# Performance work log

Measured on AMD Instinct MI355X. Metric: run time of the kernel, lower is better.

The kernel has to match this reference:

```python
import jax, jax.numpy as jnp
import numpy as np

N = 50000       # nodes
E = 1200000     # edges (before self-loops)
IN_CH = 128
HID = 64
L = 3           # FAConv layers
EPS_RES = 0.1   # FAConv eps residual weight
BN_EPS = 1e-5


def _bn(x, g, b):
    # BatchNorm1d, training-mode statistics (biased variance, like torch)
    mu = x.mean(axis=0)
    var = x.var(axis=0)
    return g * (x - mu) * jax.lax.rsqrt(var + BN_EPS) + b


def setup_inputs() -> dict:
    key = jax.random.key(0)
    ks = jax.random.split(key, 12)
    s = lambda d: 1.0 / np.sqrt(d)
    H2 = HID // 2
    return {
        "x": jax.random.normal(ks[0], (N, IN_CH), jnp.float32),
        "edge_index": jax.random.randint(ks[1], (2, E), 0, N, dtype=jnp.int32),
        "batch_size": 10000,
        "W_in": jax.random.normal(ks[2], (IN_CH, HID), jnp.float32) * s(IN_CH),
        "b_in": jnp.zeros((HID,), jnp.float32),
        "att_l": jax.random.normal(ks[3], (L, HID), jnp.float32) * s(HID),
        "att_r": jax.random.normal(ks[4], (L, HID), jnp.float32) * s(HID),
        "bn_g": jnp.ones((L, HID), jnp.float32),
        "bn_b": jnp.zeros((L, HID), jnp.float32),
        "W1": jax.random.normal(ks[5], (HID, HID), jnp.float32) * s(HID),
        "b1": jnp.zeros((HID,), jnp.float32),
        "g1": jnp.ones((HID,), jnp.float32),
        "be1": jnp.zeros((HID,), jnp.float32),
        "W2": jax.random.normal(ks[6], (HID, H2), jnp.float32) * s(HID),
        "b2": jnp.zeros((H2,), jnp.float32),
        "g2": jnp.ones((H2,), jnp.float32),
        "be2": jnp.zeros((H2,), jnp.float32),
        "W3": jax.random.normal(ks[7], (H2, 1), jnp.float32) * s(H2),
        "b3": jnp.zeros((1,), jnp.float32),
    }


def reference(x, edge_index, batch_size, W_in, b_in, att_l, att_r, bn_g, bn_b,
              W1, b1, g1, be1, W2, b2, g2, be2, W3, b3):
    n = x.shape[0]
    # gcn_norm with self-loops (same for all layers since graph is fixed)
    loops = jnp.arange(n, dtype=edge_index.dtype)
    src = jnp.concatenate([edge_index[0], loops])  # j (source)
    dst = jnp.concatenate([edge_index[1], loops])  # i (target)
    deg = jax.ops.segment_sum(jnp.ones_like(dst, dtype=x.dtype), dst, num_segments=n)
    dinv = jnp.where(deg > 0, jax.lax.rsqrt(deg), 0.0)
    norm = dinv[src] * dinv[dst]                   # [E+N]

    x0 = jax.nn.relu(x @ W_in + b_in)              # [N, HID]
    h = x0
    for l in range(L):
        al = h @ att_l[l]                          # [N] att_l^T x
        ar = h @ att_r[l]                          # [N] att_r^T x
        alpha = jnp.tanh(al[src] + ar[dst])        # [E+N] signed attention
        msg = h[src] * (alpha * norm)[:, None]     # gather + weight
        out = jax.ops.segment_sum(msg, dst, num_segments=n) + EPS_RES * x0
        h = _bn(jax.nn.relu(out), bn_g[l], bn_b[l])

    z = h[:batch_size]
    z = jax.nn.relu(_bn(z @ W1 + b1, g1, be1))
    z = jax.nn.relu(_bn(z @ W2 + b2, g2, be2))
    return (z @ W3 + b3).squeeze(-1)
```

## Files before the change

kernel.cpp:

```cpp
#include <hip/hip_runtime.h>
#include <hip/hip_bf16.h>
#include <math.h>

#define NND 50000
#define NE  1200000
#define TOT (NE + NND)
#define INCH 128
#define HID 64
#define H2  32
#define NL  3
#define BSZ 10000
#define NB  196
#define NHB 128
#define NSTAT 128
#define NAGG 2048
#define CHUNK 4096
#define EPS_RES 0.1f
#define BN_EPS 1e-5f

typedef unsigned short ushort8v __attribute__((ext_vector_type(8)));
typedef unsigned short ushort4v __attribute__((ext_vector_type(4)));

__device__ __forceinline__ float b2f(unsigned short u) {
    return __uint_as_float((unsigned)u << 16);
}

__device__ __forceinline__ float fast_tanh(float x) {
    float cx = fminf(fmaxf(x, -8.f), 8.f);
    float e = __expf(2.f * cx);
    return 1.f - __fdividef(2.f, e + 1.f);
}


__global__ __launch_bounds__(256) void bhist_kernel(const int* __restrict__ dst, int* __restrict__ bh_part, int ne) {
    __shared__ int arr[256];
    arr[threadIdx.x] = 0;
    __syncthreads();
    int i = blockIdx.x * 256 + threadIdx.x;
    int stride = gridDim.x * 256;
    for (int e = i; e < ne; e += stride) atomicAdd(&arr[dst[e] >> 8], 1);
    __syncthreads();
    bh_part[blockIdx.x * 256 + threadIdx.x] = arr[threadIdx.x];
}

__global__ __launch_bounds__(256) void bscan_kernel(const int* __restrict__ bh_part,
                                                    int* __restrict__ bstart, int* __restrict__ bcur,
                                                    int* __restrict__ offsets) {
    __shared__ int ls[256];
    int t = threadIdx.x;
    int v = 0;
    for (int k = 0; k < NHB; k++) v += bh_part[k * 256 + t];
    ls[t] = v;
    __syncthreads();
    for (int off = 1; off < 256; off <<= 1) {
        int tv = (t >= off) ? ls[t - off] : 0;
        __syncthreads();
        ls[t] += tv;
        __syncthreads();
    }
    int excl = ls[t] - v;
    if (t < NB) { bstart[t] = excl; bcur[t] = excl; }
    if (t == NB) bstart[NB] = ls[NB - 1];
    if (t == 0) offsets[NND] = TOT;
}

__global__ __launch_bounds__(256) void passA_kernel(const int* __restrict__ src, const int* __restrict__ dst,
                                                    int* __restrict__ bcur, unsigned* __restrict__ ebuf, int ne) {
    __shared__ int arr[256];
    int t = threadIdx.x;
    int base = blockIdx.x * CHUNK;
    int lim = min(base + CHUNK, ne);
    arr[t] = 0;
    __syncthreads();
    for (int e = base + t; e < lim; e += 256) atomicAdd(&arr[dst[e] >> 8], 1);
    __syncthreads();
    int cnt_t = arr[t];
    int claimed = 0;
    if (cnt_t > 0) claimed = atomicAdd(&bcur[t], cnt_t);
    __syncthreads();
    arr[t] = claimed;
    __syncthreads();
    for (int e = base + t; e < lim; e += 256) {
        int d = dst[e];
        int pos = atomicAdd(&arr[d >> 8], 1);
        ebuf[pos] = ((unsigned)src[e] << 8) | (unsigned)(d & 255);
    }
}

__global__ __launch_bounds__(256) void bucket_build_kernel(const unsigned* __restrict__ ebuf, const int* __restrict__ bstart,
                                                           int* __restrict__ offsets, int* __restrict__ csr,
                                                           float* __restrict__ aldi_f) {
    __shared__ int dcnt[256];
    __shared__ int ls[256];
    __shared__ int cur[256];
    int b = blockIdx.x, t = threadIdx.x;
    dcnt[t] = 0;
    __syncthreads();
    int beg = bstart[b], end = bstart[b + 1];
    for (int p = beg + t; p < end; p += 256) atomicAdd(&dcnt[ebuf[p] & 255u], 1);
    __syncthreads();
    int node = b * 256 + t;
    bool valid = node < NND;
    int d = valid ? (dcnt[t] + 1) : 0;
    ls[t] = d;
    __syncthreads();
    for (int off = 1; off < 256; off <<= 1) {
        int tv = (t >= off) ? ls[t - off] : 0;
        __syncthreads();
        ls[t] += tv;
        __syncthreads();
    }
    int off = bstart[b] + b * 256 + ls[t] - d;
    if (valid) {
        offsets[node] = off;
        aldi_f[2 * node + 1] = rsqrtf((float)d);
        csr[off] = node;
        cur[t] = off + 1;
    }
    __syncthreads();
    for (int p = beg + t; p < end; p += 256) {
        unsigned ed = ebuf[p];
        int pos = atomicAdd(&cur[ed & 255u], 1);
        csr[pos] = (int)(ed >> 8);
    }
}

__global__ __launch_bounds__(256) void gemm_in_kernel(const float* __restrict__ x, const float* __restrict__ W,
                                                      const float* __restrict__ b,
                                                      const float* __restrict__ attl, const float* __restrict__ attr,
                                                      __hip_bfloat16* __restrict__ x0bf,
                                                      float* __restrict__ aldi_f, float* __restrict__ ar) {
    __shared__ float Wl[INCH * HID];
    __shared__ float xs[16 * INCH];
    int t = threadIdx.x;
    for (int i = t; i < INCH * HID; i += 256) Wl[i] = W[i];
    size_t rowbase = (size_t)blockIdx.x * 16;
    for (int i = t; i < 16 * INCH; i += 256) xs[i] = x[rowbase * INCH + i];
    __syncthreads();
    int col = t & 63, rg = t >> 6;
    float a0 = 0.f, a1 = 0.f, a2 = 0.f, a3 = 0.f;
    for (int k = 0; k < INCH; k++) {
        float wk = Wl[k * HID + col];
        a0 = fmaf(xs[(rg * 4 + 0) * INCH + k], wk, a0);
        a1 = fmaf(xs[(rg * 4 + 1) * INCH + k], wk, a1);
        a2 = fmaf(xs[(rg * 4 + 2) * INCH + k], wk, a2);
        a3 = fmaf(xs[(rg * 4 + 3) * INCH + k], wk, a3);
    }
    float bb = b[col];
    a0 = fmaxf(a0 + bb, 0.f); a1 = fmaxf(a1 + bb, 0.f);
    a2 = fmaxf(a2 + bb, 0.f); a3 = fmaxf(a3 + bb, 0.f);
    size_t r = rowbase + rg * 4;
    x0bf[(r + 0) * HID + col] = __float2bfloat16(a0);
    x0bf[(r + 1) * HID + col] = __float2bfloat16(a1);
    x0bf[(r + 2) * HID + col] = __float2bfloat16(a2);
    x0bf[(r + 3) * HID + col] = __float2bfloat16(a3);
    float wl = attl[col], wr = attr[col];
    float p0 = a0 * wl, q0 = a0 * wr, p1 = a1 * wl, q1 = a1 * wr;
    float p2 = a2 * wl, q2 = a2 * wr, p3 = a3 * wl, q3 = a3 * wr;
    for (int off = 32; off > 0; off >>= 1) {
        p0 += __shfl_xor(p0, off); q0 += __shfl_xor(q0, off);
        p1 += __shfl_xor(p1, off); q1 += __shfl_xor(q1, off);
        p2 += __shfl_xor(p2, off); q2 += __shfl_xor(q2, off);
        p3 += __shfl_xor(p3, off); q3 += __shfl_xor(q3, off);
    }
    if (col == 0) {
        aldi_f[2 * (r + 0)] = p0; ar[r + 0] = q0;
        aldi_f[2 * (r + 1)] = p1; ar[r + 1] = q1;
        aldi_f[2 * (r + 2)] = p2; ar[r + 2] = q2;
        aldi_f[2 * (r + 3)] = p3; ar[r + 3] = q3;
    }
}

__global__ __launch_bounds__(256) void aggregate_kernel(const __hip_bfloat16* __restrict__ hbf,
                                                        const __hip_bfloat16* __restrict__ x0bf,
                                                        const float2* __restrict__ aldi,
                                                        const float* __restrict__ ar,
                                                        const int* __restrict__ offsets, const int* __restrict__ csr,
                                                        float* __restrict__ y, int n) {
    int wave = threadIdx.x >> 6;
    int lane = threadIdx.x & 63;
    int g = lane >> 3;
    int cl = (lane & 7) << 3;
    const unsigned short* hb = (const unsigned short*)hbf;
    for (int vb = blockIdx.x; (vb << 2) < n; vb += gridDim.x) {
        int v = (vb << 2) + wave;
        if (v >= n) continue;
        int beg = offsets[v], end = offsets[v + 1];
        float arv = ar[v];
        float a0 = 0.f, a1 = 0.f, a2 = 0.f, a3 = 0.f, a4 = 0.f, a5 = 0.f, a6 = 0.f, a7 = 0.f;
        for (int base = beg; base < end; base += 64) {
            int p = base + lane;
            int u = 0; float c = 0.f;
            if (p < end) {
                u = csr[p];
                float2 ad = aldi[u];
                c = fast_tanh(ad.x + arv) * ad.y;
            }
            int cnt = min(64, end - base);
            int nchunk = (cnt + 31) >> 5;
            for (int ch = 0; ch < nchunk; ++ch) {
                int j0 = (ch << 5) + g;
                int j1 = j0 + 8, j2 = j0 + 16, j3 = j0 + 24;
                int js0 = (j0 < cnt) ? j0 : 0;
                int js1 = (j1 < cnt) ? j1 : 0;
                int js2 = (j2 < cnt) ? j2 : 0;
                int js3 = (j3 < cnt) ? j3 : 0;
                int u0 = __shfl(u, js0); float c0 = __shfl(c, js0); if (j0 >= cnt) c0 = 0.f;
                int u1 = __shfl(u, js1); float c1 = __shfl(c, js1); if (j1 >= cnt) c1 = 0.f;
                int u2 = __shfl(u, js2); float c2 = __shfl(c, js2); if (j2 >= cnt) c2 = 0.f;
                int u3 = __shfl(u, js3); float c3 = __shfl(c, js3); if (j3 >= cnt) c3 = 0.f;
                ushort8v h0 = *(const ushort8v*)(hb + (size_t)u0 * HID + cl);
                ushort8v h1 = *(const ushort8v*)(hb + (size_t)u1 * HID + cl);
                ushort8v h2 = *(const ushort8v*)(hb + (size_t)u2 * HID + cl);
                ushort8v h3 = *(const ushort8v*)(hb + (size_t)u3 * HID + cl);
                a0 = fmaf(b2f(h0[0]), c0, a0); a1 = fmaf(b2f(h0[1]), c0, a1);
                a2 = fmaf(b2f(h0[2]), c0, a2); a3 = fmaf(b2f(h0[3]), c0, a3);
                a4 = fmaf(b2f(h0[4]), c0, a4); a5 = fmaf(b2f(h0[5]), c0, a5);
                a6 = fmaf(b2f(h0[6]), c0, a6); a7 = fmaf(b2f(h0[7]), c0, a7);
                a0 = fmaf(b2f(h1[0]), c1, a0); a1 = fmaf(b2f(h1[1]), c1, a1);
                a2 = fmaf(b2f(h1[2]), c1, a2); a3 = fmaf(b2f(h1[3]), c1, a3);
                a4 = fmaf(b2f(h1[4]), c1, a4); a5 = fmaf(b2f(h1[5]), c1, a5);
                a6 = fmaf(b2f(h1[6]), c1, a6); a7 = fmaf(b2f(h1[7]), c1, a7);
                a0 = fmaf(b2f(h2[0]), c2, a0); a1 = fmaf(b2f(h2[1]), c2, a1);
                a2 = fmaf(b2f(h2[2]), c2, a2); a3 = fmaf(b2f(h2[3]), c2, a3);
                a4 = fmaf(b2f(h2[4]), c2, a4); a5 = fmaf(b2f(h2[5]), c2, a5);
                a6 = fmaf(b2f(h2[6]), c2, a6); a7 = fmaf(b2f(h2[7]), c2, a7);
                a0 = fmaf(b2f(h3[0]), c3, a0); a1 = fmaf(b2f(h3[1]), c3, a1);
                a2 = fmaf(b2f(h3[2]), c3, a2); a3 = fmaf(b2f(h3[3]), c3, a3);
                a4 = fmaf(b2f(h3[4]), c3, a4); a5 = fmaf(b2f(h3[5]), c3, a5);
                a6 = fmaf(b2f(h3[6]), c3, a6); a7 = fmaf(b2f(h3[7]), c3, a7);
            }
        }
        for (int off = 8; off < 64; off <<= 1) {
            a0 += __shfl_xor(a0, off); a1 += __shfl_xor(a1, off);
            a2 += __shfl_xor(a2, off); a3 += __shfl_xor(a3, off);
            a4 += __shfl_xor(a4, off); a5 += __shfl_xor(a5, off);
            a6 += __shfl_xor(a6, off); a7 += __shfl_xor(a7, off);
        }
        if (g == 0) {
            float dv = aldi[v].y;
            ushort8v xb = *(const ushort8v*)((const unsigned short*)x0bf + (size_t)v * HID + cl);
            float4 o0, o1;
            o0.x = fmaxf(fmaf(EPS_RES, b2f(xb[0]), a0 * dv), 0.f);
            o0.y = fmaxf(fmaf(EPS_RES, b2f(xb[1]), a1 * dv), 0.f);
            o0.z = fmaxf(fmaf(EPS_RES, b2f(xb[2]), a2 * dv), 0.f);
            o0.w = fmaxf(fmaf(EPS_RES, b2f(xb[3]), a3 * dv), 0.f);
            o1.x = fmaxf(fmaf(EPS_RES, b2f(xb[4]), a4 * dv), 0.f);
            o1.y = fmaxf(fmaf(EPS_RES, b2f(xb[5]), a5 * dv), 0.f);
            o1.z = fmaxf(fmaf(EPS_RES, b2f(xb[6]), a6 * dv), 0.f);
            o1.w = fmaxf(fmaf(EPS_RES, b2f(xb[7]), a7 * dv), 0.f);
            *(float4*)(y + (size_t)v * HID + cl) = o0;
            *(float4*)(y + (size_t)v * HID + cl + 4) = o1;
        }
    }
}

template <int C>
__global__ __launch_bounds__(256) void bn_stats_fused_kernel(const float* __restrict__ y, int rows,
                                                             const float* __restrict__ g, const float* __restrict__ b,
                                                             float rows_inv,
                                                             float* __restrict__ acc, int* __restrict__ counter,
                                                             float* __restrict__ scale, float* __restrict__ shift) {
    const int TPR = C / 4;
    const int RPW = 64 / TPR;
    int lane = threadIdx.x & 63;
    int wave = threadIdx.x >> 6;
    int cl = (lane % TPR) * 4;
    int rsub = lane / TPR;
    int rpb = 4 * RPW;
    int r = blockIdx.x * rpb + wave * RPW + rsub;
    int stride = gridDim.x * rpb;
    float s0 = 0.f, s1 = 0.f, s2 = 0.f, s3 = 0.f, q0 = 0.f, q1 = 0.f, q2 = 0.f, q3 = 0.f;
    for (; r < rows; r += stride) {
        float4 v = *(const float4*)(y + (size_t)r * C + cl);
        s0 += v.x; q0 = fmaf(v.x, v.x, q0);
        s1 += v.y; q1 = fmaf(v.y, v.y, q1);
        s2 += v.z; q2 = fmaf(v.z, v.z, q2);
        s3 += v.w; q3 = fmaf(v.w, v.w, q3);
    }
    for (int off = TPR; off < 64; off <<= 1) {
        s0 += __shfl_xor(s0, off); q0 += __shfl_xor(q0, off);
        s1 += __shfl_xor(s1, off); q1 += __shfl_xor(q1, off);
        s2 += __shfl_xor(s2, off); q2 += __shfl_xor(q2, off);
        s3 += __shfl_xor(s3, off); q3 += __shfl_xor(q3, off);
    }
    __shared__ float lsum[4][64], lsq[4][64];
    if (lane < TPR) {
        lsum[wave][cl + 0] = s0; lsq[wave][cl + 0] = q0;
        lsum[wave][cl + 1] = s1; lsq[wave][cl + 1] = q1;
        lsum[wave][cl + 2] = s2; lsq[wave][cl + 2] = q2;
        lsum[wave][cl + 3] = s3; lsq[wave][cl + 3] = q3;
    }
    __syncthreads();
    int t = threadIdx.x;
    if (t < C) {
        float ts = lsum[0][t] + lsum[1][t] + lsum[2][t] + lsum[3][t];
        float tq = lsq[0][t] + lsq[1][t] + lsq[2][t] + lsq[3][t];
        atomicAdd(&acc[t], ts);
        atomicAdd(&acc[64 + t], tq);
    }
    __shared__ int islast;
    __syncthreads();
    if (t == 0) {
        __threadfence();
        int old = atomicAdd(counter, 1);
        islast = (old == (int)gridDim.x - 1) ? 1 : 0;
    }
    __syncthreads();
    if (islast && t < C) {
        float ts = atomicAdd(&acc[t], 0.f);
        float tq = atomicAdd(&acc[64 + t], 0.f);
        float mean = ts * rows_inv;
        float var = tq * rows_inv - mean * mean;
        float sc = g[t] * rsqrtf(var + BN_EPS);
        scale[t] = sc;
        shift[t] = b[t] - mean * sc;
    }
}

__global__ __launch_bounds__(256) void bnapply_attn_kernel(const float* __restrict__ y, const float* __restrict__ scale,
                                                           const float* __restrict__ shift,
                                                           const float* __restrict__ attl, const float* __restrict__ attr,
                                                           __hip_bfloat16* __restrict__ hbf,
                                                           float* __restrict__ aldi_f, float* __restrict__ arr_out, int n) {
    int lane = threadIdx.x & 63;
    int wave = threadIdx.x >> 6;
    int rsub = lane >> 4;
    int cl = (lane & 15) << 2;
    int r = blockIdx.x * 16 + wave * 4 + rsub;
    if (r >= n) return;
    float4 v = *(const float4*)(y + (size_t)r * HID + cl);
    float4 sc = *(const float4*)(scale + cl);
    float4 sh = *(const float4*)(shift + cl);
    float v0 = fmaf(v.x, sc.x, sh.x);
    float v1 = fmaf(v.y, sc.y, sh.y);
    float v2 = fmaf(v.z, sc.z, sh.z);
    float v3 = fmaf(v.w, sc.w, sh.w);
    __hip_bfloat16 b0 = __float2bfloat16(v0), b1 = __float2bfloat16(v1);
    __hip_bfloat16 b2 = __float2bfloat16(v2), b3 = __float2bfloat16(v3);
    ushort4v hv;
    hv[0] = *(unsigned short*)&b0; hv[1] = *(unsigned short*)&b1;
    hv[2] = *(unsigned short*)&b2; hv[3] = *(unsigned short*)&b3;
    *(ushort4v*)((unsigned short*)hbf + (size_t)r * HID + cl) = hv;
    float4 wl4 = *(const float4*)(attl + cl);
    float4 wr4 = *(const float4*)(attr + cl);
    float pl = v0 * wl4.x + v1 * wl4.y + v2 * wl4.z + v3 * wl4.w;
    float pr = v0 * wr4.x + v1 * wr4.y + v2 * wr4.z + v3 * wr4.w;
    for (int off = 1; off < 16; off <<= 1) {
        pl += __shfl_xor(pl, off);
        pr += __shfl_xor(pr, off);
    }
    if ((lane & 15) == 0) { aldi_f[2 * r] = pl; arr_out[r] = pr; }
}

__global__ __launch_bounds__(256) void mlp1_kernel(const float* __restrict__ y, const float* __restrict__ scale,
                                                   const float* __restrict__ shift, const float* __restrict__ W,
                                                   const float* __restrict__ b, float* __restrict__ z1) {
    __shared__ float Wl[HID * HID];
    __shared__ float xs[16 * HID];
    int t = threadIdx.x;
    for (int i = t; i < HID * HID; i += 256) Wl[i] = W[i];
    size_t rowbase = (size_t)blockIdx.x * 16;
    for (int i = t; i < 16 * HID; i += 256) {
        int c = i & 63;
        xs[i] = fmaf(y[rowbase * HID + i], scale[c], shift[c]);
    }
    __syncthreads();
    int col = t & 63, rg = t >> 6;
    float a0 = 0.f, a1 = 0.f, a2 = 0.f, a3 = 0.f;
    for (int k = 0; k < HID; k++) {
        float wk = Wl[k * HID + col];
        a0 = fmaf(xs[(rg * 4 + 0) * HID + k], wk, a0);
        a1 = fmaf(xs[(rg * 4 + 1) * HID + k], wk, a1);
        a2 = fmaf(xs[(rg * 4 + 2) * HID + k], wk, a2);
        a3 = fmaf(xs[(rg * 4 + 3) * HID + k], wk, a3);
    }
    float bb = b[col];
    size_t r = rowbase + rg * 4;
    z1[(r + 0) * HID + col] = a0 + bb;
    z1[(r + 1) * HID + col] = a1 + bb;
    z1[(r + 2) * HID + col] = a2 + bb;
    z1[(r + 3) * HID + col] = a3 + bb;
}

__global__ __launch_bounds__(256) void mlp2_kernel(const float* __restrict__ z1, const float* __restrict__ scale,
                                                   const float* __restrict__ shift, const float* __restrict__ W,
                                                   const float* __restrict__ b, float* __restrict__ z2) {
    __shared__ float Wl[HID * H2];
    __shared__ float as[16 * HID];
    int t = threadIdx.x;
    for (int i = t; i < HID * H2; i += 256) Wl[i] = W[i];
    size_t rowbase = (size_t)blockIdx.x * 16;
    for (int i = t; i < 16 * HID; i += 256) {
        int c = i & 63;
        float v = z1[rowbase * HID + i];
        as[i] = fmaxf(fmaf(v, scale[c], shift[c]), 0.f);
    }
    __syncthreads();
    int col = t & 31, rg = t >> 5;
    float a0 = 0.f, a1 = 0.f;
    for (int k = 0; k < HID; k++) {
        float wk = Wl[k * H2 + col];
        a0 = fmaf(as[(rg * 2 + 0) * HID + k], wk, a0);
        a1 = fmaf(as[(rg * 2 + 1) * HID + k], wk, a1);
    }
    float bb = b[col];
    size_t r = rowbase + rg * 2;
    z2[(r + 0) * H2 + col] = a0 + bb;
    z2[(r + 1) * H2 + col] = a1 + bb;
}

__global__ __launch_bounds__(256) void mlp3_kernel(const float* __restrict__ z2, const float* __restrict__ scale,
                                                   const float* __restrict__ shift, const float* __restrict__ W3,
                                                   const float* __restrict__ b3, float* __restrict__ out, int rows) {
    int i = blockIdx.x * 256 + threadIdx.x;
    if (i >= rows) return;
    float acc = 0.f;
#pragma unroll
    for (int k = 0; k < H2; k++) {
        float v = fmaxf(fmaf(z2[(size_t)i * H2 + k], scale[k], shift[k]), 0.f);
        acc = fmaf(v, W3[k], acc);
    }
    out[i] = acc + b3[0];
}

extern "C" void kernel_launch(void* const* d_in, const int* in_sizes, int n_in,
                              void* d_out, int out_size, void* d_ws, size_t ws_size,
                              hipStream_t stream) {
    const float* x     = (const float*)d_in[0];
    const int*   ei    = (const int*)d_in[1];
    const int*   src   = ei;
    const int*   dst   = ei + NE;
    const float* W_in  = (const float*)d_in[3];
    const float* b_in  = (const float*)d_in[4];
    const float* att_l = (const float*)d_in[5];
    const float* att_r = (const float*)d_in[6];
    const float* bn_g  = (const float*)d_in[7];
    const float* bn_b  = (const float*)d_in[8];
    const float* W1    = (const float*)d_in[9];
    const float* b1    = (const float*)d_in[10];
    const float* g1    = (const float*)d_in[11];
    const float* be1   = (const float*)d_in[12];
    const float* W2    = (const float*)d_in[13];
    const float* b2    = (const float*)d_in[14];
    const float* g2    = (const float*)d_in[15];
    const float* be2   = (const float*)d_in[16];
    const float* W3    = (const float*)d_in[17];
    const float* b3    = (const float*)d_in[18];
    float* out = (float*)d_out;

    char* p = (char*)d_ws;
    auto carve = [&](size_t bytes) -> void* {
        void* r = (void*)p;
        p += (bytes + 255) & ~(size_t)255;
        return r;
    };
    int*   bh_part = (int*)carve((size_t)NHB * 256 * 4);
    int*   bstart  = (int*)carve(256 * 4);
    int*   bcur    = (int*)carve(256 * 4);
    int*   offsets = (int*)carve((size_t)(NND + 1) * 4);
    int*   csr     = (int*)carve((size_t)TOT * 4);
    float2* aldi   = (float2*)carve((size_t)NND * 8);
    float* ar      = (float*)carve((size_t)NND * 4);
    __hip_bfloat16* x0bf = (__hip_bfloat16*)carve((size_t)NND * HID * 2);
    __hip_bfloat16* hbfA = (__hip_bfloat16*)carve((size_t)NND * HID * 2);
    __hip_bfloat16* hbfB = (__hip_bfloat16*)carve((size_t)NND * HID * 2);
    float* ybuf    = (float*)carve((size_t)NND * HID * 4);
    unsigned* ebuf = (unsigned*)ybuf;
    float* accall  = (float*)carve(5 * 256 * 4);
    float* scale   = (float*)carve(64 * 4);
    float* shift   = (float*)carve(64 * 4);
    float* z1      = (float*)carve((size_t)BSZ * HID * 4);
    float* z2      = (float*)carve((size_t)BSZ * H2 * 4);

    auto accr = [&](int i) -> float* { return accall + i * 256; };
    auto ctr  = [&](int i) -> int*   { return (int*)(accall + i * 256 + 128); };

    const int nblkA = (NE + CHUNK - 1) / CHUNK;

    hipMemsetAsync(accall, 0, 5 * 256 * 4, stream);

    bhist_kernel<<<NHB, 256, 0, stream>>>(dst, bh_part, NE);
    gemm_in_kernel<<<NND / 16, 256, 0, stream>>>(x, W_in, b_in, att_l, att_r, x0bf, (float*)aldi, ar);
    bscan_kernel<<<1, 256, 0, stream>>>(bh_part, bstart, bcur, offsets);
    passA_kernel<<<nblkA, 256, 0, stream>>>(src, dst, bcur, ebuf, NE);
    bucket_build_kernel<<<NB, 256, 0, stream>>>(ebuf, bstart, offsets, csr, (float*)aldi);

    const __hip_bfloat16* h_in = x0bf;
    __hip_bfloat16* hbufs[2] = {hbfA, hbfB};
    for (int l = 0; l < NL; l++) {
        aggregate_kernel<<<NAGG, 256, 0, stream>>>(h_in, x0bf, aldi, ar, offsets, csr, ybuf, NND);
        bn_stats_fused_kernel<64><<<NSTAT, 256, 0, stream>>>(ybuf, NND, bn_g + l * HID, bn_b + l * HID,
                                                             1.0f / NND, accr(l), ctr(l), scale, shift);
        if (l < NL - 1) {
            bnapply_attn_kernel<<<(NND + 15) / 16, 256, 0, stream>>>(ybuf, scale, shift,
                                                                     att_l + (l + 1) * HID, att_r + (l + 1) * HID,
                                                                     hbufs[l], (float*)aldi, ar, NND);
            h_in = hbufs[l];
        }
    }

    mlp1_kernel<<<BSZ / 16, 256, 0, stream>>>(ybuf, scale, shift, W1, b1, z1);
    bn_stats_fused_kernel<64><<<NSTAT, 256, 0, stream>>>(z1, BSZ, g1, be1, 1.0f / BSZ, accr(3), ctr(3), scale, shift);

    mlp2_kernel<<<BSZ / 16, 256, 0, stream>>>(z1, scale, shift, W2, b2, z2);
    bn_stats_fused_kernel<32><<<NSTAT, 256, 0, stream>>>(z2, BSZ, g2, be2, 1.0f / BSZ, accr(4), ctr(4), scale, shift);

    mlp3_kernel<<<(BSZ + 255) / 256, 256, 0, stream>>>(z2, scale, shift, W3, b3, out, BSZ);
}
```

Baseline: 365.5 us.

## Fuse BatchNorm statistics into producer kernels and finalize in consumers

Removes the separate BN-statistics kernels. The aggregate and MLP kernels now accumulate per-column sums and sums of squares in registers and shared memory, then atomically add them to a global accumulator. Each consumer kernel (bnapply, mlp1/2/3) recomputes scale and shift from those sums in shared memory. This saves five launches and a full re-read of the y/z buffers, at the cost of extra registers in aggregate and redundant per-block finalization.

```diff
diff --git a/kernel.cpp b/kernel.cpp
--- a/kernel.cpp
+++ b/kernel.cpp
@@ -12,7 +12,6 @@
 #define BSZ 10000
 #define NB  196
 #define NHB 128
-#define NSTAT 128
 #define NAGG 2048
 #define CHUNK 4096
 #define EPS_RES 0.1f
@@ -176,12 +175,15 @@
                                                         const float2* __restrict__ aldi,
                                                         const float* __restrict__ ar,
                                                         const int* __restrict__ offsets, const int* __restrict__ csr,
-                                                        float* __restrict__ y, int n) {
+                                                        float* __restrict__ y, float* __restrict__ acc, int n) {
+    __shared__ float lsum[4][64], lsq[4][64];
     int wave = threadIdx.x >> 6;
     int lane = threadIdx.x & 63;
     int g = lane >> 3;
     int cl = (lane & 7) << 3;
     const unsigned short* hb = (const unsigned short*)hbf;
+    float rs0 = 0.f, rs1 = 0.f, rs2 = 0.f, rs3 = 0.f, rs4 = 0.f, rs5 = 0.f, rs6 = 0.f, rs7 = 0.f;
+    float rq0 = 0.f, rq1 = 0.f, rq2 = 0.f, rq3 = 0.f, rq4 = 0.f, rq5 = 0.f, rq6 = 0.f, rq7 = 0.f;
     for (int vb = blockIdx.x; (vb << 2) < n; vb += gridDim.x) {
         int v = (vb << 2) + wave;
         if (v >= n) continue;
@@ -251,91 +253,64 @@
             o1.w = fmaxf(fmaf(EPS_RES, b2f(xb[7]), a7 * dv), 0.f);
             *(float4*)(y + (size_t)v * HID + cl) = o0;
             *(float4*)(y + (size_t)v * HID + cl + 4) = o1;
+            rs0 += o0.x; rq0 = fmaf(o0.x, o0.x, rq0);
+            rs1 += o0.y; rq1 = fmaf(o0.y, o0.y, rq1);
+            rs2 += o0.z; rq2 = fmaf(o0.z, o0.z, rq2);
+            rs3 += o0.w; rq3 = fmaf(o0.w, o0.w, rq3);
+            rs4 += o1.x; rq4 = fmaf(o1.x, o1.x, rq4);
+            rs5 += o1.y; rq5 = fmaf(o1.y, o1.y, rq5);
+            rs6 += o1.z; rq6 = fmaf(o1.z, o1.z, rq6);
+            rs7 += o1.w; rq7 = fmaf(o1.w, o1.w, rq7);
         }
     }
-}
-
-template <int C>
-__global__ __launch_bounds__(256) void bn_stats_fused_kernel(const float* __restrict__ y, int rows,
-                                                             const float* __restrict__ g, const float* __restrict__ b,
-                                                             float rows_inv,
-                                                             float* __restrict__ acc, int* __restrict__ counter,
-                                                             float* __restrict__ scale, float* __restrict__ shift) {
-    const int TPR = C / 4;
-    const int RPW = 64 / TPR;
-    int lane = threadIdx.x & 63;
-    int wave = threadIdx.x >> 6;
-    int cl = (lane % TPR) * 4;
-    int rsub = lane / TPR;
-    int rpb = 4 * RPW;
-    int r = blockIdx.x * rpb + wave * RPW + rsub;
-    int stride = gridDim.x * rpb;
-    float s0 = 0.f, s1 = 0.f, s2 = 0.f, s3 = 0.f, q0 = 0.f, q1 = 0.f, q2 = 0.f, q3 = 0.f;
-    for (; r < rows; r += stride) {
-        float4 v = *(const float4*)(y + (size_t)r * C + cl);
-        s0 += v.x; q0 = fmaf(v.x, v.x, q0);
-        s1 += v.y; q1 = fmaf(v.y, v.y, q1);
-        s2 += v.z; q2 = fmaf(v.z, v.z, q2);
-        s3 += v.w; q3 = fmaf(v.w, v.w, q3);
-    }
-    for (int off = TPR; off < 64; off <<= 1) {
-        s0 += __shfl_xor(s0, off); q0 += __shfl_xor(q0, off);
-        s1 += __shfl_xor(s1, off); q1 += __shfl_xor(q1, off);
-        s2 += __shfl_xor(s2, off); q2 += __shfl_xor(q2, off);
-        s3 += __shfl_xor(s3, off); q3 += __shfl_xor(q3, off);
-    }
-    __shared__ float lsum[4][64], lsq[4][64];
-    if (lane < TPR) {
-        lsum[wave][cl + 0] = s0; lsq[wave][cl + 0] = q0;
-        lsum[wave][cl + 1] = s1; lsq[wave][cl + 1] = q1;
-        lsum[wave][cl + 2] = s2; lsq[wave][cl + 2] = q2;
-        lsum[wave][cl + 3] = s3; lsq[wave][cl + 3] = q3;
-    }
-    __syncthreads();
-    int t = threadIdx.x;
-    if (t < C) {
-        float ts = lsum[0][t] + lsum[1][t] + lsum[2][t] + lsum[3][t];
-        float tq = lsq[0][t] + lsq[1][t] + lsq[2][t] + lsq[3][t];
-        atomicAdd(&acc[t], ts);
-        atomicAdd(&acc[64 + t], tq);
-    }
-    __shared__ int islast;
-    __syncthreads();
-    if (t == 0) {
-        __threadfence();
-        int old = atomicAdd(counter, 1);
-        islast = (old == (int)gridDim.x - 1) ? 1 : 0;
-    }
-    __syncthreads();
-    if (islast && t < C) {
-        float ts = atomicAdd(&acc[t], 0.f);
-        float tq = atomicAdd(&acc[64 + t], 0.f);
+    if (g == 0) {
+        lsum[wave][cl + 0] = rs0; lsq[wave][cl + 0] = rq0;
+        lsum[wave][cl + 1] = rs1; lsq[wave][cl + 1] = rq1;
+        lsum[wave][cl + 2] = rs2; lsq[wave][cl + 2] = rq2;
+        lsum[wave][cl + 3] = rs3; lsq[wave][cl + 3] = rq3;
+        lsum[wave][cl + 4] = rs4; lsq[wave][cl + 4] = rq4;
+        lsum[wave][cl + 5] = rs5; lsq[wave][cl + 5] = rq5;
+        lsum[wave][cl + 6] = rs6; lsq[wave][cl + 6] = rq6;
+        lsum[wave][cl + 7] = rs7; lsq[wave][cl + 7] = rq7;
+    }
+    __syncthreads();
+    int t = threadIdx.x;
+    if (t < 64) {
+        float s = lsum[0][t] + lsum[1][t] + lsum[2][t] + lsum[3][t];
+        float q = lsq[0][t] + lsq[1][t] + lsq[2][t] + lsq[3][t];
+        atomicAdd(&acc[t], s);
+        atomicAdd(&acc[64 + t], q);
+    }
+}
+
+__global__ __launch_bounds__(256) void bnapply_attn_kernel(const float* __restrict__ y,
+                                                           const float* __restrict__ acc, float rows_inv,
+                                                           const float* __restrict__ g, const float* __restrict__ b,
+                                                           const float* __restrict__ attl, const float* __restrict__ attr,
+                                                           __hip_bfloat16* __restrict__ hbf,
+                                                           float* __restrict__ aldi_f, float* __restrict__ arr_out, int n) {
+    __shared__ float s_sc[64], s_sh[64];
+    int t = threadIdx.x;
+    if (t < 64) {
+        float ts = acc[t], tq = acc[64 + t];
         float mean = ts * rows_inv;
         float var = tq * rows_inv - mean * mean;
         float sc = g[t] * rsqrtf(var + BN_EPS);
-        scale[t] = sc;
-        shift[t] = b[t] - mean * sc;
-    }
-}
-
-__global__ __launch_bounds__(256) void bnapply_attn_kernel(const float* __restrict__ y, const float* __restrict__ scale,
-                                                           const float* __restrict__ shift,
-                                                           const float* __restrict__ attl, const float* __restrict__ attr,
-                                                           __hip_bfloat16* __restrict__ hbf,
-                                                           float* __restrict__ aldi_f, float* __restrict__ arr_out, int n) {
-    int lane = threadIdx.x & 63;
-    int wave = threadIdx.x >> 6;
+        s_sc[t] = sc;
+        s_sh[t] = b[t] - mean * sc;
+    }
+    __syncthreads();
+    int lane = t & 63;
+    int wave = t >> 6;
     int rsub = lane >> 4;
     int cl = (lane & 15) << 2;
     int r = blockIdx.x * 16 + wave * 4 + rsub;
     if (r >= n) return;
     float4 v = *(const float4*)(y + (size_t)r * HID + cl);
-    float4 sc = *(const float4*)(scale + cl);
-    float4 sh = *(const float4*)(shift + cl);
-    float v0 = fmaf(v.x, sc.x, sh.x);
-    float v1 = fmaf(v.y, sc.y, sh.y);
-    float v2 = fmaf(v.z, sc.z, sh.z);
-    float v3 = fmaf(v.w, sc.w, sh.w);
+    float v0 = fmaf(v.x, s_sc[cl + 0], s_sh[cl + 0]);
+    float v1 = fmaf(v.y, s_sc[cl + 1], s_sh[cl + 1]);
+    float v2 = fmaf(v.z, s_sc[cl + 2], s_sh[cl + 2]);
+    float v3 = fmaf(v.w, s_sc[cl + 3], s_sh[cl + 3]);
     __hip_bfloat16 b0 = __float2bfloat16(v0), b1 = __float2bfloat16(v1);
     __hip_bfloat16 b2 = __float2bfloat16(v2), b3 = __float2bfloat16(v3);
     ushort4v hv;
@@ -353,17 +328,30 @@
     if ((lane & 15) == 0) { aldi_f[2 * r] = pl; arr_out[r] = pr; }
 }
 
-__global__ __launch_bounds__(256) void mlp1_kernel(const float* __restrict__ y, const float* __restrict__ scale,
-                                                   const float* __restrict__ shift, const float* __restrict__ W,
-                                                   const float* __restrict__ b, float* __restrict__ z1) {
+__global__ __launch_bounds__(256) void mlp1_kernel(const float* __restrict__ y,
+                                                   const float* __restrict__ acc_in, float rows_inv_in,
+                                                   const float* __restrict__ gin, const float* __restrict__ bin,
+                                                   const float* __restrict__ W, const float* __restrict__ b,
+                                                   float* __restrict__ z1, float* __restrict__ acc_out) {
     __shared__ float Wl[HID * HID];
     __shared__ float xs[16 * HID];
-    int t = threadIdx.x;
+    __shared__ float s_sc[64], s_sh[64];
+    __shared__ float zs[4][64], zq[4][64];
+    int t = threadIdx.x;
+    if (t < 64) {
+        float ts = acc_in[t], tq = acc_in[64 + t];
+        float mean = ts * rows_inv_in;
+        float var = tq * rows_inv_in - mean * mean;
+        float sc = gin[t] * rsqrtf(var + BN_EPS);
+        s_sc[t] = sc;
+        s_sh[t] = bin[t] - mean * sc;
+    }
     for (int i = t; i < HID * HID; i += 256) Wl[i] = W[i];
+    __syncthreads();
     size_t rowbase = (size_t)blockIdx.x * 16;
     for (int i = t; i < 16 * HID; i += 256) {
         int c = i & 63;
-        xs[i] = fmaf(y[rowbase * HID + i], scale[c], shift[c]);
+        xs[i] = fmaf(y[rowbase * HID + i], s_sc[c], s_sh[c]);
     }
     __syncthreads();
     int col = t & 63, rg = t >> 6;
@@ -376,25 +364,48 @@
         a3 = fmaf(xs[(rg * 4 + 3) * HID + k], wk, a3);
     }
     float bb = b[col];
+    a0 += bb; a1 += bb; a2 += bb; a3 += bb;
     size_t r = rowbase + rg * 4;
-    z1[(r + 0) * HID + col] = a0 + bb;
-    z1[(r + 1) * HID + col] = a1 + bb;
-    z1[(r + 2) * HID + col] = a2 + bb;
-    z1[(r + 3) * HID + col] = a3 + bb;
-}
-
-__global__ __launch_bounds__(256) void mlp2_kernel(const float* __restrict__ z1, const float* __restrict__ scale,
-                                                   const float* __restrict__ shift, const float* __restrict__ W,
-                                                   const float* __restrict__ b, float* __restrict__ z2) {
+    z1[(r + 0) * HID + col] = a0;
+    z1[(r + 1) * HID + col] = a1;
+    z1[(r + 2) * HID + col] = a2;
+    z1[(r + 3) * HID + col] = a3;
+    zs[rg][col] = a0 + a1 + a2 + a3;
+    zq[rg][col] = a0 * a0 + a1 * a1 + a2 * a2 + a3 * a3;
+    __syncthreads();
+    if (t < 64) {
+        float s = zs[0][t] + zs[1][t] + zs[2][t] + zs[3][t];
+        float q = zq[0][t] + zq[1][t] + zq[2][t] + zq[3][t];
+        atomicAdd(&acc_out[t], s);
+        atomicAdd(&acc_out[64 + t], q);
+    }
+}
+
+__global__ __launch_bounds__(256) void mlp2_kernel(const float* __restrict__ z1,
+                                                   const float* __restrict__ acc_in, float rows_inv_in,
+                                                   const float* __restrict__ gin, const float* __restrict__ bin,
+                                                   const float* __restrict__ W, const float* __restrict__ b,
+                                                   float* __restrict__ z2, float* __restrict__ acc_out) {
     __shared__ float Wl[HID * H2];
     __shared__ float as[16 * HID];
-    int t = threadIdx.x;
+    __shared__ float s_sc[64], s_sh[64];
+    __shared__ float zs[8][32], zq[8][32];
+    int t = threadIdx.x;
+    if (t < 64) {
+        float ts = acc_in[t], tq = acc_in[64 + t];
+        float mean = ts * rows_inv_in;
+        float var = tq * rows_inv_in - mean * mean;
+        float sc = gin[t] * rsqrtf(var + BN_EPS);
+        s_sc[t] = sc;
+        s_sh[t] = bin[t] - mean * sc;
+    }
     for (int i = t; i < HID * H2; i += 256) Wl[i] = W[i];
+    __syncthreads();
     size_t rowbase = (size_t)blockIdx.x * 16;
     for (int i = t; i < 16 * HID; i += 256) {
         int c = i & 63;
         float v = z1[rowbase * HID + i];
-        as[i] = fmaxf(fmaf(v, scale[c], shift[c]), 0.f);
+        as[i] = fmaxf(fmaf(v, s_sc[c], s_sh[c]), 0.f);
     }
     __syncthreads();
     int col = t & 31, rg = t >> 5;
@@ -405,20 +416,44 @@
         a1 = fmaf(as[(rg * 2 + 1) * HID + k], wk, a1);
     }
     float bb = b[col];
+    a0 += bb; a1 += bb;
     size_t r = rowbase + rg * 2;
-    z2[(r + 0) * H2 + col] = a0 + bb;
-    z2[(r + 1) * H2 + col] = a1 + bb;
-}
-
-__global__ __launch_bounds__(256) void mlp3_kernel(const float* __restrict__ z2, const float* __restrict__ scale,
-                                                   const float* __restrict__ shift, const float* __restrict__ W3,
-                                                   const float* __restrict__ b3, float* __restrict__ out, int rows) {
-    int i = blockIdx.x * 256 + threadIdx.x;
+    z2[(r + 0) * H2 + col] = a0;
+    z2[(r + 1) * H2 + col] = a1;
+    zs[rg][col] = a0 + a1;
+    zq[rg][col] = a0 * a0 + a1 * a1;
+    __syncthreads();
+    if (t < 32) {
+        float s = 0.f, q = 0.f;
+#pragma unroll
+        for (int w = 0; w < 8; w++) { s += zs[w][t]; q += zq[w][t]; }
+        atomicAdd(&acc_out[t], s);
+        atomicAdd(&acc_out[64 + t], q);
+    }
+}
+
+__global__ __launch_bounds__(256) void mlp3_kernel(const float* __restrict__ z2,
+                                                   const float* __restrict__ acc_in, float rows_inv_in,
+                                                   const float* __restrict__ gin, const float* __restrict__ bin,
+                                                   const float* __restrict__ W3, const float* __restrict__ b3,
+                                                   float* __restrict__ out, int rows) {
+    __shared__ float s_sc[32], s_sh[32];
+    int t = threadIdx.x;
+    if (t < 32) {
+        float ts = acc_in[t], tq = acc_in[64 + t];
+        float mean = ts * rows_inv_in;
+        float var = tq * rows_inv_in - mean * mean;
+        float sc = gin[t] * rsqrtf(var + BN_EPS);
+        s_sc[t] = sc;
+        s_sh[t] = bin[t] - mean * sc;
+    }
+    __syncthreads();
+    int i = blockIdx.x * 256 + t;
     if (i >= rows) return;
     float acc = 0.f;
 #pragma unroll
     for (int k = 0; k < H2; k++) {
-        float v = fmaxf(fmaf(z2[(size_t)i * H2 + k], scale[k], shift[k]), 0.f);
+        float v = fmaxf(fmaf(z2[(size_t)i * H2 + k], s_sc[k], s_sh[k]), 0.f);
         acc = fmaf(v, W3[k], acc);
     }
     out[i] = acc + b3[0];
@@ -468,13 +503,10 @@
     float* ybuf    = (float*)carve((size_t)NND * HID * 4);
     unsigned* ebuf = (unsigned*)ybuf;
     float* accall  = (float*)carve(5 * 256 * 4);
-    float* scale   = (float*)carve(64 * 4);
-    float* shift   = (float*)carve(64 * 4);
     float* z1      = (float*)carve((size_t)BSZ * HID * 4);
     float* z2      = (float*)carve((size_t)BSZ * H2 * 4);
 
     auto accr = [&](int i) -> float* { return accall + i * 256; };
-    auto ctr  = [&](int i) -> int*   { return (int*)(accall + i * 256 + 128); };
 
     const int nblkA = (NE + CHUNK - 1) / CHUNK;
 
@@ -489,22 +521,18 @@
     const __hip_bfloat16* h_in = x0bf;
     __hip_bfloat16* hbufs[2] = {hbfA, hbfB};
     for (int l = 0; l < NL; l++) {
-        aggregate_kernel<<<NAGG, 256, 0, stream>>>(h_in, x0bf, aldi, ar, offsets, csr, ybuf, NND);
-        bn_stats_fused_kernel<64><<<NSTAT, 256, 0, stream>>>(ybuf, NND, bn_g + l * HID, bn_b + l * HID,
-                                                             1.0f / NND, accr(l), ctr(l), scale, shift);
+        aggregate_kernel<<<NAGG, 256, 0, stream>>>(h_in, x0bf, aldi, ar, offsets, csr, ybuf, accr(l), NND);
         if (l < NL - 1) {
-            bnapply_attn_kernel<<<(NND + 15) / 16, 256, 0, stream>>>(ybuf, scale, shift,
+            bnapply_attn_kernel<<<(NND + 15) / 16, 256, 0, stream>>>(ybuf, accr(l), 1.0f / NND,
+                                                                     bn_g + l * HID, bn_b + l * HID,
                                                                      att_l + (l + 1) * HID, att_r + (l + 1) * HID,
                                                                      hbufs[l], (float*)aldi, ar, NND);
             h_in = hbufs[l];
         }
     }
 
-    mlp1_kernel<<<BSZ / 16, 256, 0, stream>>>(ybuf, scale, shift, W1, b1, z1);
-    bn_stats_fused_kernel<64><<<NSTAT, 256, 0, stream>>>(z1, BSZ, g1, be1, 1.0f / BSZ, accr(3), ctr(3), scale, shift);
-
-    mlp2_kernel<<<BSZ / 16, 256, 0, stream>>>(z1, scale, shift, W2, b2, z2);
-    bn_stats_fused_kernel<32><<<NSTAT, 256, 0, stream>>>(z2, BSZ, g2, be2, 1.0f / BSZ, accr(4), ctr(4), scale, shift);
-
-    mlp3_kernel<<<(BSZ + 255) / 256, 256, 0, stream>>>(z2, scale, shift, W3, b3, out, BSZ);
-}
+    mlp1_kernel<<<BSZ / 16, 256, 0, stream>>>(ybuf, accr(2), 1.0f / NND, bn_g + 2 * HID, bn_b + 2 * HID,
+                                              W1, b1, z1, accr(3));
+    mlp2_kernel<<<BSZ / 16, 256, 0, stream>>>(z1, accr(3), 1.0f / BSZ, g1, be1, W2, b2, z2, accr(4));
+    mlp3_kernel<<<(BSZ + 255) / 256, 256, 0, stream>>>(z2, accr(4), 1.0f / BSZ, g2, be2, W3, b3, out, BSZ);
+}
```

Measured after the change: 448.9 us. +22.8%, slower.

## Split each wave into two half-waves to aggregate two nodes concurrently

Applied to the files above, without the earlier changes.

The aggregation kernel now assigns two destination nodes per wave, one per 32-lane half, so each block covers eight nodes instead of four. Neighbor lists are processed in strides of 32 edges, with shuffles offset into the owning half and a reduction over 32 lanes only. The aim is less lane waste on low-degree nodes (average degree about 25), where a full 64-lane chunk was mostly idle. The cost is that both halves loop to the larger of their two stride counts, so the wave can diverge when the halves have very different degrees.

```diff
diff --git a/kernel.cpp b/kernel.cpp
--- a/kernel.cpp
+++ b/kernel.cpp
@@ -179,36 +179,42 @@
                                                         float* __restrict__ y, int n) {
     int wave = threadIdx.x >> 6;
     int lane = threadIdx.x & 63;
-    int g = lane >> 3;
-    int cl = (lane & 7) << 3;
+    int half = lane >> 5;
+    int ll   = lane & 31;
+    int sg   = ll >> 3;
+    int cl   = (ll & 7) << 3;
+    int hbase = half << 5;
     const unsigned short* hb = (const unsigned short*)hbf;
-    for (int vb = blockIdx.x; (vb << 2) < n; vb += gridDim.x) {
-        int v = (vb << 2) + wave;
-        if (v >= n) continue;
-        int beg = offsets[v], end = offsets[v + 1];
-        float arv = ar[v];
+    for (int vb = blockIdx.x; (vb << 3) < n; vb += gridDim.x) {
+        int v = (vb << 3) + (wave << 1) + half;
+        bool vvalid = v < n;
+        int beg = 0, end = 0;
+        float arv = 0.f;
+        if (vvalid) { beg = offsets[v]; end = offsets[v + 1]; arv = ar[v]; }
+        int nstr = (end - beg + 31) >> 5;
+        int mstr = max(nstr, __shfl_xor(nstr, 32));
         float a0 = 0.f, a1 = 0.f, a2 = 0.f, a3 = 0.f, a4 = 0.f, a5 = 0.f, a6 = 0.f, a7 = 0.f;
-        for (int base = beg; base < end; base += 64) {
-            int p = base + lane;
+        for (int s = 0; s < mstr; ++s) {
+            int sb = beg + (s << 5);
+            int p = sb + ll;
             int u = 0; float c = 0.f;
             if (p < end) {
                 u = csr[p];
                 float2 ad = aldi[u];
                 c = fast_tanh(ad.x + arv) * ad.y;
             }
-            int cnt = min(64, end - base);
-            int nchunk = (cnt + 31) >> 5;
-            for (int ch = 0; ch < nchunk; ++ch) {
-                int j0 = (ch << 5) + g;
-                int j1 = j0 + 8, j2 = j0 + 16, j3 = j0 + 24;
+            int cnt = end - sb;
+            for (int ch = 0; ch < 2; ++ch) {
+                int j0 = (ch << 4) + sg;
+                int j1 = j0 + 4, j2 = j0 + 8, j3 = j0 + 12;
                 int js0 = (j0 < cnt) ? j0 : 0;
                 int js1 = (j1 < cnt) ? j1 : 0;
                 int js2 = (j2 < cnt) ? j2 : 0;
                 int js3 = (j3 < cnt) ? j3 : 0;
-                int u0 = __shfl(u, js0); float c0 = __shfl(c, js0); if (j0 >= cnt) c0 = 0.f;
-                int u1 = __shfl(u, js1); float c1 = __shfl(c, js1); if (j1 >= cnt) c1 = 0.f;
-                int u2 = __shfl(u, js2); float c2 = __shfl(c, js2); if (j2 >= cnt) c2 = 0.f;
-                int u3 = __shfl(u, js3); float c3 = __shfl(c, js3); if (j3 >= cnt) c3 = 0.f;
+                int u0 = __shfl(u, hbase + js0); float c0 = __shfl(c, hbase + js0); if (j0 >= cnt) c0 = 0.f;
+                int u1 = __shfl(u, hbase + js1); float c1 = __shfl(c, hbase + js1); if (j1 >= cnt) c1 = 0.f;
+                int u2 = __shfl(u, hbase + js2); float c2 = __shfl(c, hbase + js2); if (j2 >= cnt) c2 = 0.f;
+                int u3 = __shfl(u, hbase + js3); float c3 = __shfl(c, hbase + js3); if (j3 >= cnt) c3 = 0.f;
                 ushort8v h0 = *(const ushort8v*)(hb + (size_t)u0 * HID + cl);
                 ushort8v h1 = *(const ushort8v*)(hb + (size_t)u1 * HID + cl);
                 ushort8v h2 = *(const ushort8v*)(hb + (size_t)u2 * HID + cl);
@@ -231,13 +237,13 @@
                 a6 = fmaf(b2f(h3[6]), c3, a6); a7 = fmaf(b2f(h3[7]), c3, a7);
             }
         }
-        for (int off = 8; off < 64; off <<= 1) {
+        for (int off = 8; off < 32; off <<= 1) {
             a0 += __shfl_xor(a0, off); a1 += __shfl_xor(a1, off);
             a2 += __shfl_xor(a2, off); a3 += __shfl_xor(a3, off);
             a4 += __shfl_xor(a4, off); a5 += __shfl_xor(a5, off);
             a6 += __shfl_xor(a6, off); a7 += __shfl_xor(a7, off);
         }
-        if (g == 0) {
+        if (sg == 0 && vvalid) {
             float dv = aldi[v].y;
             ushort8v xb = *(const ushort8v*)((const unsigned short*)x0bf + (size_t)v * HID + cl);
             float4 o0, o1;
```

After: 347.9 us. 4.8% less time.
